# Kernel tuning notes

Hardware: AMD Instinct MI355X
Metric: run time of the kernel (lower is better)

## Reference

```python
import jax, jax.numpy as jnp
import numpy as np

N = 50000
E = 800000
IN_DIM, HID_DIM, LAT_DIM, OUT_DIM = 128, 128, 64, 128
NEG_SLOPE = 0.2  # PyG GATConv default


def setup_inputs() -> dict:
    key = jax.random.key(0)
    ks = jax.random.split(key, 24)
    def glorot(k, shape):
        lim = float(np.sqrt(6.0 / (shape[0] + shape[-1])))
        return jax.random.uniform(k, shape, jnp.float32, -lim, lim)
    inp = {
        "x": jax.random.normal(ks[0], (N, IN_DIM), jnp.float32),
        "edge_index": jax.random.randint(ks[1], (2, E), 0, N, jnp.int32),
        "eps": jax.random.normal(ks[2], (N, LAT_DIM), jnp.float32),
        # GATConv 1 (heads=1)
        "W1": glorot(ks[3], (IN_DIM, HID_DIM)),
        "a_src1": glorot(ks[4], (HID_DIM,)),
        "a_dst1": glorot(ks[5], (HID_DIM,)),
        "b1": jnp.zeros((HID_DIM,), jnp.float32),
        # GATConv 2
        "W2": glorot(ks[6], (HID_DIM, LAT_DIM)),
        "a_src2": glorot(ks[7], (LAT_DIM,)),
        "a_dst2": glorot(ks[8], (LAT_DIM,)),
        "b2": jnp.zeros((LAT_DIM,), jnp.float32),
        # VAE heads
        "W_mu": glorot(ks[9], (LAT_DIM, LAT_DIM)),
        "b_mu": jnp.zeros((LAT_DIM,), jnp.float32),
        "W_lv": glorot(ks[10], (LAT_DIM, LAT_DIM)),
        "b_lv": jnp.zeros((LAT_DIM,), jnp.float32),
        "W_d1": glorot(ks[11], (LAT_DIM, HID_DIM)),
        "b_d1": jnp.zeros((HID_DIM,), jnp.float32),
        "W_d2": glorot(ks[12], (HID_DIM, OUT_DIM)),
        "b_d2": jnp.zeros((OUT_DIM,), jnp.float32),
    }
    return inp


def gat_conv(x, W, a_src, a_dst, b, src, dst):
    # x: [N, F_in] -> h: [N, F_out]
    h = x @ W
    # per-node attention halves (single head)
    alpha_s = h @ a_src           # [N]
    alpha_d = h @ a_dst           # [N]
    # per-edge score: leaky_relu(a_src . h_j + a_dst . h_i), edge j->i
    e = jax.nn.leaky_relu(alpha_s[src] + alpha_d[dst], NEG_SLOPE)  # [E']
    # scatter-softmax over incoming edges of each destination node
    m = jax.ops.segment_max(e, dst, num_segments=N)                # [N]
    ex = jnp.exp(e - m[dst])
    denom = jax.ops.segment_sum(ex, dst, num_segments=N)           # [N]
    w = ex / denom[dst]                                            # [E']
    # scatter-add weighted messages
    out = jax.ops.segment_sum(h[src] * w[:, None], dst, num_segments=N)
    return out + b


def reference(x, edge_index, eps, W1, a_src1, a_dst1, b1, W2, a_src2, a_dst2, b2,
              W_mu, b_mu, W_lv, b_lv, W_d1, b_d1, W_d2, b_d2):
    # add self loops (PyG GATConv default add_self_loops=True)
    loops = jnp.arange(N, dtype=edge_index.dtype)
    src = jnp.concatenate([edge_index[0], loops])
    dst = jnp.concatenate([edge_index[1], loops])

    h = jax.nn.relu(gat_conv(x, W1, a_src1, a_dst1, b1, src, dst))
    h = jax.nn.relu(gat_conv(h, W2, a_src2, a_dst2, b2, src, dst))
    mu = h @ W_mu + b_mu
    logvar = h @ W_lv + b_lv
    z = mu + eps * jnp.exp(0.5 * logvar)
    d = jax.nn.relu(z @ W_d1 + b_d1)
    recon_x = jax.nn.sigmoid(d @ W_d2 + b_d2)
    return recon_x, mu, logvar
```

## Files before the change

kernel.cpp:

```cpp
#include <hip/hip_runtime.h>
#include <stdint.h>

typedef unsigned int u32;

__device__ __forceinline__ float lrelu(float x){ return x > 0.f ? x : 0.2f*x; }

__global__ void k_hist(const int* __restrict__ dst, int* __restrict__ deg, int E){
  int e = blockIdx.x*blockDim.x + threadIdx.x;
  if (e < E) atomicAdd(&deg[dst[e]], 1);
}

__global__ void k_scan1(const int* __restrict__ deg, int* __restrict__ offs,
                        int* __restrict__ bsum, int n){
  __shared__ int lds[256];
  int t = threadIdx.x;
  int base = blockIdx.x*1024 + t*4;
  int v0 = (base+0<n)?deg[base+0]:0;
  int v1 = (base+1<n)?deg[base+1]:0;
  int v2 = (base+2<n)?deg[base+2]:0;
  int v3 = (base+3<n)?deg[base+3]:0;
  int s = v0+v1+v2+v3;
  lds[t] = s; __syncthreads();
  for (int off=1; off<256; off<<=1){
    int tmp = (t>=off)? lds[t-off] : 0;
    __syncthreads();
    lds[t] += tmp;
    __syncthreads();
  }
  int excl = lds[t] - s;
  if (t==255) bsum[blockIdx.x] = lds[255];
  if (base+0<n) offs[base+0] = excl;
  if (base+1<n) offs[base+1] = excl+v0;
  if (base+2<n) offs[base+2] = excl+v0+v1;
  if (base+3<n) offs[base+3] = excl+v0+v1+v2;
}

__global__ void k_scan2(int* bsum, int nb){
  int lane = threadIdx.x;
  int v = (lane<nb)? bsum[lane] : 0;
  int orig = v;
  for (int off=1; off<64; off<<=1){
    int t = __shfl_up(v, off);
    if (lane >= off) v += t;
  }
  if (lane<nb) bsum[lane] = v - orig;
}

__global__ void k_scan3(int* __restrict__ offs, int* __restrict__ cur,
                        const int* __restrict__ bsum, int n){
  int i = blockIdx.x*blockDim.x + threadIdx.x;
  if (i<n){ int v = offs[i] + bsum[i>>10]; offs[i]=v; cur[i]=v; }
}

__global__ void k_scatter(const int* __restrict__ src, const int* __restrict__ dst,
                          int* __restrict__ cur, int* __restrict__ adj, int E){
  int e = blockIdx.x*blockDim.x + threadIdx.x;
  if (e<E){
    int d = dst[e];
    int p = atomicAdd(&cur[d], 1);
    adj[p] = src[e];
  }
}

template<int FOUT>
__global__ void k_gemm(const float* __restrict__ X, const float* __restrict__ W,
                       float* __restrict__ H, int N){
  constexpr int FIN = 128, ROWS = 16;
  __shared__ float xs[ROWS*FIN];
  int t = threadIdx.x;
  long i0 = (long)blockIdx.x*ROWS;
  {
    const float4* xsrc = (const float4*)(X + i0*FIN);
    float4 a = xsrc[t];
    float4 b = xsrc[t+256];
    ((float4*)xs)[t]     = a;
    ((float4*)xs)[t+256] = b;
  }
  __syncthreads();
  constexpr int G = 256/FOUT;
  constexpr int RPT = ROWS/G;
  int c = t % FOUT, g = t / FOUT;
  float acc[RPT];
  #pragma unroll
  for (int r=0;r<RPT;r++) acc[r]=0.f;
  for (int k=0;k<FIN;k+=4){
    float w0 = W[(k+0)*FOUT+c];
    float w1 = W[(k+1)*FOUT+c];
    float w2 = W[(k+2)*FOUT+c];
    float w3 = W[(k+3)*FOUT+c];
    #pragma unroll
    for (int r=0;r<RPT;r++){
      const float4 xv = *(const float4*)&xs[(g*RPT+r)*FIN+k];
      acc[r] = fmaf(xv.w, w3, fmaf(xv.z, w2, fmaf(xv.y, w1, fmaf(xv.x, w0, acc[r]))));
    }
  }
  #pragma unroll
  for (int r=0;r<RPT;r++)
    H[(i0 + g*RPT + r)*FOUT + c] = acc[r];
}

template<int F>
__global__ void k_alpha(const float* __restrict__ H, const float* __restrict__ Asrc,
                        const float* __restrict__ Adst, float* __restrict__ AS,
                        float* __restrict__ AD, int N){
  int lane = threadIdx.x & 63;
  int i = blockIdx.x*4 + (threadIdx.x >> 6);
  if (i >= N) return;
  float as = 0.f, ad = 0.f;
  #pragma unroll
  for (int c = lane; c < F; c += 64){
    float hv = H[(long)i*F + c];
    as = fmaf(hv, Asrc[c], as);
    ad = fmaf(hv, Adst[c], ad);
  }
  #pragma unroll
  for (int off=32; off; off>>=1){
    as += __shfl_xor(as, off);
    ad += __shfl_xor(ad, off);
  }
  if (lane==0){ AS[i]=as; AD[i]=ad; }
}

template<int F>
__global__ void k_agg(const float* __restrict__ H, const float* __restrict__ AS,
                      const float* __restrict__ AD, const float* __restrict__ B,
                      const int* __restrict__ offs, const int* __restrict__ deg,
                      const int* __restrict__ adj, float* __restrict__ OUT, int N){
  int lane = threadIdx.x & 63;
  int i = blockIdx.x*4 + (threadIdx.x >> 6);
  if (i >= N) return;
  int start = offs[i], dg = deg[i];
  float ad = AD[i];
  float lr_self = lrelu(AS[i] + ad);
  float m = -1e30f, dacc = 0.f;
  for (int b0=0; b0<dg; b0+=64){
    int k = b0 + lane;
    if (k < dg){
      int s = adj[start+k];
      float lr = lrelu(AS[s] + ad);
      float mn = fmaxf(m, lr);
      dacc = dacc*__expf(m-mn) + __expf(lr-mn);
      m = mn;
    }
  }
  #pragma unroll
  for (int off=32; off; off>>=1){
    float m2 = __shfl_xor(m, off);
    float d2 = __shfl_xor(dacc, off);
    float mn = fmaxf(m, m2);
    dacc = dacc*__expf(m-mn) + d2*__expf(m2-mn);
    m = mn;
  }
  float M = fmaxf(m, lr_self);
  float D = dacc*__expf(m-M) + __expf(lr_self-M);
  float invD = 1.f/D;
  float wself = __expf(lr_self-M)*invD;
  float acc0 = wself * H[(long)i*F + lane];
  float acc1 = 0.f;
  if (F==128) acc1 = wself * H[(long)i*F + 64 + lane];
  for (int b0=0; b0<dg; b0+=64){
    int k = b0 + lane;
    int sreg = 0; float wreg = 0.f;
    if (k < dg){
      sreg = adj[start+k];
      wreg = __expf(lrelu(AS[sreg]+ad) - M)*invD;
    }
    int cnt = min(64, dg-b0);
    int kk = 0;
    for (; kk+4<=cnt; kk+=4){
      int   s0=__shfl(sreg,kk),   s1=__shfl(sreg,kk+1),   s2=__shfl(sreg,kk+2),   s3=__shfl(sreg,kk+3);
      float w0=__shfl(wreg,kk),   w1=__shfl(wreg,kk+1),   w2=__shfl(wreg,kk+2),   w3=__shfl(wreg,kk+3);
      float h0 = H[(long)s0*F+lane];
      float h1 = H[(long)s1*F+lane];
      float h2 = H[(long)s2*F+lane];
      float h3 = H[(long)s3*F+lane];
      acc0 += w0*h0 + w1*h1 + w2*h2 + w3*h3;
      if (F==128){
        float g0 = H[(long)s0*F+64+lane];
        float g1 = H[(long)s1*F+64+lane];
        float g2 = H[(long)s2*F+64+lane];
        float g3 = H[(long)s3*F+64+lane];
        acc1 += w0*g0 + w1*g1 + w2*g2 + w3*g3;
      }
    }
    for (; kk<cnt; kk++){
      int s0=__shfl(sreg,kk); float w0=__shfl(wreg,kk);
      acc0 += w0*H[(long)s0*F+lane];
      if (F==128) acc1 += w0*H[(long)s0*F+64+lane];
    }
  }
  float o0 = fmaxf(acc0 + B[lane], 0.f);
  OUT[(long)i*F+lane] = o0;
  if (F==128){
    float o1 = fmaxf(acc1 + B[64+lane], 0.f);
    OUT[(long)i*F+64+lane] = o1;
  }
}

__global__ void k_head(const float* __restrict__ H2, const float* __restrict__ EPS,
                       const float* __restrict__ Wmu, const float* __restrict__ bmu,
                       const float* __restrict__ Wlv, const float* __restrict__ blv,
                       const float* __restrict__ Wd1, const float* __restrict__ bd1,
                       const float* __restrict__ Wd2, const float* __restrict__ bd2,
                       float* __restrict__ out_recon, float* __restrict__ out_mu,
                       float* __restrict__ out_lv, int N){
  constexpr int ROWS=16;
  __shared__ float h2s[ROWS*64];
  __shared__ float zs[ROWS*64];
  __shared__ float ds[ROWS*128];
  int t = threadIdx.x;
  long i0 = (long)blockIdx.x*ROWS;
  {
    const float4* s4 = (const float4*)(H2 + i0*64);
    ((float4*)h2s)[t] = s4[t];
  }
  __syncthreads();
  {
    int c = t & 63, q = t >> 6;
    float am[4] = {0,0,0,0}, av[4] = {0,0,0,0};
    for (int k=0;k<64;k++){
      float wm = Wmu[k*64+c];
      float wv = Wlv[k*64+c];
      #pragma unroll
      for (int r=0;r<4;r++){
        float h = h2s[(q*4+r)*64 + k];
        am[r] = fmaf(h, wm, am[r]);
        av[r] = fmaf(h, wv, av[r]);
      }
    }
    float bm = bmu[c], bv = blv[c];
    #pragma unroll
    for (int r=0;r<4;r++){
      int row = q*4+r; long i = i0 + row;
      float mu = am[r] + bm;
      float lv = av[r] + bv;
      out_mu[i*64+c] = mu;
      out_lv[i*64+c] = lv;
      zs[row*64+c] = fmaf(EPS[i*64+c], __expf(0.5f*lv), mu);
    }
  }
  __syncthreads();
  {
    int c = t & 127, q = t >> 7;
    float accd[8] = {0,0,0,0,0,0,0,0};
    for (int k=0;k<64;k++){
      float w = Wd1[k*128+c];
      #pragma unroll
      for (int r=0;r<8;r++)
        accd[r] = fmaf(zs[(q*8+r)*64+k], w, accd[r]);
    }
    float bb = bd1[c];
    #pragma unroll
    for (int r=0;r<8;r++)
      ds[(q*8+r)*128+c] = fmaxf(accd[r]+bb, 0.f);
  }
  __syncthreads();
  {
    int c = t & 127, q = t >> 7;
    float accr[8] = {0,0,0,0,0,0,0,0};
    for (int k=0;k<128;k++){
      float w = Wd2[k*128+c];
      #pragma unroll
      for (int r=0;r<8;r++)
        accr[r] = fmaf(ds[(q*8+r)*128+k], w, accr[r]);
    }
    float bb = bd2[c];
    #pragma unroll
    for (int r=0;r<8;r++){
      long i = i0 + q*8 + r;
      float v = accr[r] + bb;
      out_recon[i*128+c] = 1.f/(1.f+__expf(-v));
    }
  }
}

extern "C" void kernel_launch(void* const* d_in, const int* in_sizes, int n_in,
                              void* d_out, int out_size, void* d_ws, size_t ws_size,
                              hipStream_t stream){
  const float* x    = (const float*)d_in[0];
  const int*   ei   = (const int*)  d_in[1];
  const float* eps  = (const float*)d_in[2];
  const float* W1   = (const float*)d_in[3];
  const float* as1v = (const float*)d_in[4];
  const float* ad1v = (const float*)d_in[5];
  const float* b1   = (const float*)d_in[6];
  const float* W2   = (const float*)d_in[7];
  const float* as2v = (const float*)d_in[8];
  const float* ad2v = (const float*)d_in[9];
  const float* b2   = (const float*)d_in[10];
  const float* Wmu  = (const float*)d_in[11];
  const float* bmu  = (const float*)d_in[12];
  const float* Wlv  = (const float*)d_in[13];
  const float* blv  = (const float*)d_in[14];
  const float* Wd1  = (const float*)d_in[15];
  const float* bd1  = (const float*)d_in[16];
  const float* Wd2  = (const float*)d_in[17];
  const float* bd2  = (const float*)d_in[18];

  const int N = in_sizes[0] / 128;
  const int E = in_sizes[1] / 2;
  const int* esrc = ei;
  const int* edst = ei + E;

  char* wp = (char*)d_ws;
  auto alloc = [&](size_t bytes)->char*{
    char* p = wp; wp += (bytes + 255) & ~(size_t)255; return p;
  };
  int*   deg  = (int*)  alloc((size_t)N*4);
  int*   offs = (int*)  alloc((size_t)N*4);
  int*   cur  = (int*)  alloc((size_t)N*4);
  int*   bsum = (int*)  alloc(256*4);
  int*   adj  = (int*)  alloc((size_t)E*4);
  float* h1   = (float*)alloc((size_t)N*128*4);
  float* o1   = (float*)alloc((size_t)N*128*4);
  float* AS1  = (float*)alloc((size_t)N*4);
  float* AD1  = (float*)alloc((size_t)N*4);
  float* AS2  = (float*)alloc((size_t)N*4);
  float* AD2  = (float*)alloc((size_t)N*4);
  float* h2 = h1;
  float* o2 = h1 + (size_t)N*64;
  (void)ws_size; (void)n_in; (void)out_size;

  float* out_recon = (float*)d_out;
  float* out_mu    = out_recon + (size_t)N*128;
  float* out_lv    = out_mu    + (size_t)N*64;

  hipMemsetAsync(deg, 0, (size_t)N*4, stream);
  int eb = (E + 255)/256;
  int nb = (N + 1023)/1024;
  k_hist   <<<eb, 256, 0, stream>>>(edst, deg, E);
  k_scan1  <<<nb, 256, 0, stream>>>(deg, offs, bsum, N);
  k_scan2  <<<1,   64, 0, stream>>>(bsum, nb);
  k_scan3  <<<(N+255)/256, 256, 0, stream>>>(offs, cur, bsum, N);
  k_scatter<<<eb, 256, 0, stream>>>(esrc, edst, cur, adj, E);

  int gb = N/16;
  int wb = (N+3)/4;
  k_gemm<128> <<<gb, 256, 0, stream>>>(x, W1, h1, N);
  k_alpha<128><<<wb, 256, 0, stream>>>(h1, as1v, ad1v, AS1, AD1, N);
  k_agg<128>  <<<wb, 256, 0, stream>>>(h1, AS1, AD1, b1, offs, deg, adj, o1, N);
  k_gemm<64>  <<<gb, 256, 0, stream>>>(o1, W2, h2, N);
  k_alpha<64> <<<wb, 256, 0, stream>>>(h2, as2v, ad2v, AS2, AD2, N);
  k_agg<64>   <<<wb, 256, 0, stream>>>(h2, AS2, AD2, b2, offs, deg, adj, o2, N);
  k_head      <<<gb, 256, 0, stream>>>(o2, eps, Wmu, bmu, Wlv, blv, Wd1, bd1, Wd2, bd2,
                                       out_recon, out_mu, out_lv, N);
}
```

Before: 443.0 us.

## Register-tile dense GEMMs and VAE head with weights staged in LDS

Rewrites the node-feature GEMM and the fused VAE head so each thread computes a 4-row by 4-column register tile. Weights are staged once per block in shared memory and read as float4, and row tiles grow to 32/64 rows per block. The head now runs with 512 threads and computes mu and logvar together as one 128-wide GEMM. This cuts repeated global weight loads and raises FMA-to-load ratio. In exchange it uses much more LDS per block (about 112KB in the head), which may limit occupancy.

```diff
diff --git a/kernel.cpp b/kernel.cpp
--- a/kernel.cpp
+++ b/kernel.cpp
@@ -63,40 +63,59 @@
 }
 
 template<int FOUT>
-__global__ void k_gemm(const float* __restrict__ X, const float* __restrict__ W,
-                       float* __restrict__ H, int N){
-  constexpr int FIN = 128, ROWS = 16;
-  __shared__ float xs[ROWS*FIN];
+__global__ __launch_bounds__(256) void k_gemm_t(const float* __restrict__ X,
+                                                const float* __restrict__ W,
+                                                float* __restrict__ H, int N){
+  constexpr int CG = FOUT/4;
+  constexpr int RG = 256/CG;
+  constexpr int TR = RG*4;
+  __shared__ float xs[TR*128];
+  __shared__ float ws[128*FOUT];
   int t = threadIdx.x;
-  long i0 = (long)blockIdx.x*ROWS;
-  {
-    const float4* xsrc = (const float4*)(X + i0*FIN);
-    float4 a = xsrc[t];
-    float4 b = xsrc[t+256];
-    ((float4*)xs)[t]     = a;
-    ((float4*)xs)[t+256] = b;
-  }
-  __syncthreads();
-  constexpr int G = 256/FOUT;
-  constexpr int RPT = ROWS/G;
-  int c = t % FOUT, g = t / FOUT;
-  float acc[RPT];
-  #pragma unroll
-  for (int r=0;r<RPT;r++) acc[r]=0.f;
-  for (int k=0;k<FIN;k+=4){
-    float w0 = W[(k+0)*FOUT+c];
-    float w1 = W[(k+1)*FOUT+c];
-    float w2 = W[(k+2)*FOUT+c];
-    float w3 = W[(k+3)*FOUT+c];
-    #pragma unroll
-    for (int r=0;r<RPT;r++){
-      const float4 xv = *(const float4*)&xs[(g*RPT+r)*FIN+k];
-      acc[r] = fmaf(xv.w, w3, fmaf(xv.z, w2, fmaf(xv.y, w1, fmaf(xv.x, w0, acc[r]))));
-    }
-  }
-  #pragma unroll
-  for (int r=0;r<RPT;r++)
-    H[(i0 + g*RPT + r)*FOUT + c] = acc[r];
+  long i0 = (long)blockIdx.x * TR;
+  {
+    constexpr int NV = TR*32/256;
+    #pragma unroll
+    for (int j=0;j<NV;j++){
+      int idx = t + 256*j;
+      int row = idx >> 5, c4 = idx & 31;
+      float4 v = make_float4(0.f,0.f,0.f,0.f);
+      if (i0 + row < N) v = *(const float4*)&X[(i0+row)*128 + c4*4];
+      *(float4*)&xs[row*128 + c4*4] = v;
+    }
+  }
+  {
+    constexpr int NW = 128*FOUT/4/256;
+    const float4* Wv = (const float4*)W;
+    float4* wd = (float4*)ws;
+    #pragma unroll
+    for (int j=0;j<NW;j++) wd[t + 256*j] = Wv[t + 256*j];
+  }
+  __syncthreads();
+  int ci = t & (CG-1), rg = t / CG;
+  float4 a0 = make_float4(0,0,0,0), a1 = a0, a2 = a0, a3 = a0;
+  const float* xrow = &xs[(rg*4)*128];
+  #pragma unroll 8
+  for (int k=0;k<128;k++){
+    float4 w4 = *(const float4*)&ws[k*FOUT + ci*4];
+    float x0 = xrow[k];
+    float x1 = xrow[128 + k];
+    float x2 = xrow[256 + k];
+    float x3 = xrow[384 + k];
+    a0.x = fmaf(x0, w4.x, a0.x); a0.y = fmaf(x0, w4.y, a0.y);
+    a0.z = fmaf(x0, w4.z, a0.z); a0.w = fmaf(x0, w4.w, a0.w);
+    a1.x = fmaf(x1, w4.x, a1.x); a1.y = fmaf(x1, w4.y, a1.y);
+    a1.z = fmaf(x1, w4.z, a1.z); a1.w = fmaf(x1, w4.w, a1.w);
+    a2.x = fmaf(x2, w4.x, a2.x); a2.y = fmaf(x2, w4.y, a2.y);
+    a2.z = fmaf(x2, w4.z, a2.z); a2.w = fmaf(x2, w4.w, a2.w);
+    a3.x = fmaf(x3, w4.x, a3.x); a3.y = fmaf(x3, w4.y, a3.y);
+    a3.z = fmaf(x3, w4.z, a3.z); a3.w = fmaf(x3, w4.w, a3.w);
+  }
+  long ib = i0 + rg*4;
+  if (ib+0 < N) *(float4*)&H[(ib+0)*FOUT + ci*4] = a0;
+  if (ib+1 < N) *(float4*)&H[(ib+1)*FOUT + ci*4] = a1;
+  if (ib+2 < N) *(float4*)&H[(ib+2)*FOUT + ci*4] = a2;
+  if (ib+3 < N) *(float4*)&H[(ib+3)*FOUT + ci*4] = a3;
 }
 
 template<int F>
@@ -197,79 +216,151 @@
   }
 }
 
-__global__ void k_head(const float* __restrict__ H2, const float* __restrict__ EPS,
-                       const float* __restrict__ Wmu, const float* __restrict__ bmu,
-                       const float* __restrict__ Wlv, const float* __restrict__ blv,
-                       const float* __restrict__ Wd1, const float* __restrict__ bd1,
-                       const float* __restrict__ Wd2, const float* __restrict__ bd2,
-                       float* __restrict__ out_recon, float* __restrict__ out_mu,
-                       float* __restrict__ out_lv, int N){
-  constexpr int ROWS=16;
-  __shared__ float h2s[ROWS*64];
-  __shared__ float zs[ROWS*64];
-  __shared__ float ds[ROWS*128];
+__global__ __launch_bounds__(512) void k_head_t(
+    const float* __restrict__ H2, const float* __restrict__ EPS,
+    const float* __restrict__ Wmu, const float* __restrict__ bmu,
+    const float* __restrict__ Wlv, const float* __restrict__ blv,
+    const float* __restrict__ Wd1, const float* __restrict__ bd1,
+    const float* __restrict__ Wd2, const float* __restrict__ bd2,
+    float* __restrict__ out_recon, float* __restrict__ out_mu,
+    float* __restrict__ out_lv, int N){
+  __shared__ float hs[64*64];
+  __shared__ float zs[64*64];
+  __shared__ float dsb[64*128];
+  __shared__ float ws[128*128];
   int t = threadIdx.x;
-  long i0 = (long)blockIdx.x*ROWS;
-  {
-    const float4* s4 = (const float4*)(H2 + i0*64);
-    ((float4*)h2s)[t] = s4[t];
-  }
-  __syncthreads();
-  {
-    int c = t & 63, q = t >> 6;
-    float am[4] = {0,0,0,0}, av[4] = {0,0,0,0};
+  long i0 = (long)blockIdx.x * 64;
+  #pragma unroll
+  for (int j=0;j<2;j++){
+    int idx = t + 512*j;
+    int row = idx >> 4, c4 = idx & 15;
+    float4 v = make_float4(0.f,0.f,0.f,0.f);
+    if (i0 + row < N) v = *(const float4*)&H2[(i0+row)*64 + c4*4];
+    *(float4*)&hs[row*64 + c4*4] = v;
+  }
+  #pragma unroll
+  for (int j=0;j<4;j++){
+    int q = t + 512*j;
+    int k = q >> 5, c4 = q & 31;
+    float4 v;
+    if (c4 < 16) v = *(const float4*)&Wmu[k*64 + c4*4];
+    else         v = *(const float4*)&Wlv[k*64 + (c4-16)*4];
+    *(float4*)&ws[k*128 + c4*4] = v;
+  }
+  __syncthreads();
+  int ci = t & 31, rg = t >> 5;
+  float4 a0 = make_float4(0,0,0,0), a1 = a0, a2 = a0, a3 = a0;
+  {
+    const float* xrow = &hs[(rg*4)*64];
+    #pragma unroll 8
     for (int k=0;k<64;k++){
-      float wm = Wmu[k*64+c];
-      float wv = Wlv[k*64+c];
-      #pragma unroll
-      for (int r=0;r<4;r++){
-        float h = h2s[(q*4+r)*64 + k];
-        am[r] = fmaf(h, wm, am[r]);
-        av[r] = fmaf(h, wv, av[r]);
+      float4 w4 = *(const float4*)&ws[k*128 + ci*4];
+      float x0 = xrow[k], x1 = xrow[64+k], x2 = xrow[128+k], x3 = xrow[192+k];
+      a0.x=fmaf(x0,w4.x,a0.x); a0.y=fmaf(x0,w4.y,a0.y); a0.z=fmaf(x0,w4.z,a0.z); a0.w=fmaf(x0,w4.w,a0.w);
+      a1.x=fmaf(x1,w4.x,a1.x); a1.y=fmaf(x1,w4.y,a1.y); a1.z=fmaf(x1,w4.z,a1.z); a1.w=fmaf(x1,w4.w,a1.w);
+      a2.x=fmaf(x2,w4.x,a2.x); a2.y=fmaf(x2,w4.y,a2.y); a2.z=fmaf(x2,w4.z,a2.z); a2.w=fmaf(x2,w4.w,a2.w);
+      a3.x=fmaf(x3,w4.x,a3.x); a3.y=fmaf(x3,w4.y,a3.y); a3.z=fmaf(x3,w4.z,a3.z); a3.w=fmaf(x3,w4.w,a3.w);
+    }
+  }
+  bool is_mu = (ci < 16);
+  int cbase = is_mu ? ci*4 : (ci-16)*4;
+  if (!is_mu){
+    float4 bv = *(const float4*)&blv[cbase];
+    float4 acc[4] = {a0,a1,a2,a3};
+    #pragma unroll
+    for (int r=0;r<4;r++){
+      long i = i0 + rg*4 + r;
+      float4 lv = make_float4(acc[r].x+bv.x, acc[r].y+bv.y, acc[r].z+bv.z, acc[r].w+bv.w);
+      if (i < N) *(float4*)&out_lv[i*64 + cbase] = lv;
+      *(float4*)&zs[(rg*4+r)*64 + cbase] = lv;
+    }
+  }
+  __syncthreads();
+  if (is_mu){
+    float4 bv = *(const float4*)&bmu[cbase];
+    float4 acc[4] = {a0,a1,a2,a3};
+    #pragma unroll
+    for (int r=0;r<4;r++){
+      long i = i0 + rg*4 + r;
+      float4 mu = make_float4(acc[r].x+bv.x, acc[r].y+bv.y, acc[r].z+bv.z, acc[r].w+bv.w);
+      if (i < N) *(float4*)&out_mu[i*64 + cbase] = mu;
+      float4 lv = *(const float4*)&zs[(rg*4+r)*64 + cbase];
+      float4 e = make_float4(0.f,0.f,0.f,0.f);
+      if (i < N) e = *(const float4*)&EPS[i*64 + cbase];
+      float4 z;
+      z.x = fmaf(e.x, __expf(0.5f*lv.x), mu.x);
+      z.y = fmaf(e.y, __expf(0.5f*lv.y), mu.y);
+      z.z = fmaf(e.z, __expf(0.5f*lv.z), mu.z);
+      z.w = fmaf(e.w, __expf(0.5f*lv.w), mu.w);
+      *(float4*)&zs[(rg*4+r)*64 + cbase] = z;
+    }
+  }
+  {
+    const float4* Wv = (const float4*)Wd1;
+    float4* wd = (float4*)ws;
+    #pragma unroll
+    for (int j=0;j<4;j++) wd[t + 512*j] = Wv[t + 512*j];
+  }
+  __syncthreads();
+  a0 = make_float4(0,0,0,0); a1 = a0; a2 = a0; a3 = a0;
+  {
+    const float* xrow = &zs[(rg*4)*64];
+    #pragma unroll 8
+    for (int k=0;k<64;k++){
+      float4 w4 = *(const float4*)&ws[k*128 + ci*4];
+      float x0 = xrow[k], x1 = xrow[64+k], x2 = xrow[128+k], x3 = xrow[192+k];
+      a0.x=fmaf(x0,w4.x,a0.x); a0.y=fmaf(x0,w4.y,a0.y); a0.z=fmaf(x0,w4.z,a0.z); a0.w=fmaf(x0,w4.w,a0.w);
+      a1.x=fmaf(x1,w4.x,a1.x); a1.y=fmaf(x1,w4.y,a1.y); a1.z=fmaf(x1,w4.z,a1.z); a1.w=fmaf(x1,w4.w,a1.w);
+      a2.x=fmaf(x2,w4.x,a2.x); a2.y=fmaf(x2,w4.y,a2.y); a2.z=fmaf(x2,w4.z,a2.z); a2.w=fmaf(x2,w4.w,a2.w);
+      a3.x=fmaf(x3,w4.x,a3.x); a3.y=fmaf(x3,w4.y,a3.y); a3.z=fmaf(x3,w4.z,a3.z); a3.w=fmaf(x3,w4.w,a3.w);
+    }
+  }
+  __syncthreads();
+  {
+    float4 bv = *(const float4*)&bd1[ci*4];
+    float4 acc[4] = {a0,a1,a2,a3};
+    #pragma unroll
+    for (int r=0;r<4;r++){
+      float4 d;
+      d.x = fmaxf(acc[r].x+bv.x, 0.f); d.y = fmaxf(acc[r].y+bv.y, 0.f);
+      d.z = fmaxf(acc[r].z+bv.z, 0.f); d.w = fmaxf(acc[r].w+bv.w, 0.f);
+      *(float4*)&dsb[(rg*4+r)*128 + ci*4] = d;
+    }
+  }
+  {
+    const float4* Wv = (const float4*)Wd2;
+    float4* wd = (float4*)ws;
+    #pragma unroll
+    for (int j=0;j<8;j++) wd[t + 512*j] = Wv[t + 512*j];
+  }
+  __syncthreads();
+  a0 = make_float4(0,0,0,0); a1 = a0; a2 = a0; a3 = a0;
+  {
+    const float* xrow = &dsb[(rg*4)*128];
+    #pragma unroll 8
+    for (int k=0;k<128;k++){
+      float4 w4 = *(const float4*)&ws[k*128 + ci*4];
+      float x0 = xrow[k], x1 = xrow[128+k], x2 = xrow[256+k], x3 = xrow[384+k];
+      a0.x=fmaf(x0,w4.x,a0.x); a0.y=fmaf(x0,w4.y,a0.y); a0.z=fmaf(x0,w4.z,a0.z); a0.w=fmaf(x0,w4.w,a0.w);
+      a1.x=fmaf(x1,w4.x,a1.x); a1.y=fmaf(x1,w4.y,a1.y); a1.z=fmaf(x1,w4.z,a1.z); a1.w=fmaf(x1,w4.w,a1.w);
+      a2.x=fmaf(x2,w4.x,a2.x); a2.y=fmaf(x2,w4.y,a2.y); a2.z=fmaf(x2,w4.z,a2.z); a2.w=fmaf(x2,w4.w,a2.w);
+      a3.x=fmaf(x3,w4.x,a3.x); a3.y=fmaf(x3,w4.y,a3.y); a3.z=fmaf(x3,w4.z,a3.z); a3.w=fmaf(x3,w4.w,a3.w);
+    }
+  }
+  {
+    float4 bv = *(const float4*)&bd2[ci*4];
+    float4 acc[4] = {a0,a1,a2,a3};
+    #pragma unroll
+    for (int r=0;r<4;r++){
+      long i = i0 + rg*4 + r;
+      if (i < N){
+        float4 o;
+        o.x = 1.f/(1.f+__expf(-(acc[r].x+bv.x)));
+        o.y = 1.f/(1.f+__expf(-(acc[r].y+bv.y)));
+        o.z = 1.f/(1.f+__expf(-(acc[r].z+bv.z)));
+        o.w = 1.f/(1.f+__expf(-(acc[r].w+bv.w)));
+        *(float4*)&out_recon[i*128 + ci*4] = o;
       }
-    }
-    float bm = bmu[c], bv = blv[c];
-    #pragma unroll
-    for (int r=0;r<4;r++){
-      int row = q*4+r; long i = i0 + row;
-      float mu = am[r] + bm;
-      float lv = av[r] + bv;
-      out_mu[i*64+c] = mu;
-      out_lv[i*64+c] = lv;
-      zs[row*64+c] = fmaf(EPS[i*64+c], __expf(0.5f*lv), mu);
-    }
-  }
-  __syncthreads();
-  {
-    int c = t & 127, q = t >> 7;
-    float accd[8] = {0,0,0,0,0,0,0,0};
-    for (int k=0;k<64;k++){
-      float w = Wd1[k*128+c];
-      #pragma unroll
-      for (int r=0;r<8;r++)
-        accd[r] = fmaf(zs[(q*8+r)*64+k], w, accd[r]);
-    }
-    float bb = bd1[c];
-    #pragma unroll
-    for (int r=0;r<8;r++)
-      ds[(q*8+r)*128+c] = fmaxf(accd[r]+bb, 0.f);
-  }
-  __syncthreads();
-  {
-    int c = t & 127, q = t >> 7;
-    float accr[8] = {0,0,0,0,0,0,0,0};
-    for (int k=0;k<128;k++){
-      float w = Wd2[k*128+c];
-      #pragma unroll
-      for (int r=0;r<8;r++)
-        accr[r] = fmaf(ds[(q*8+r)*128+k], w, accr[r]);
-    }
-    float bb = bd2[c];
-    #pragma unroll
-    for (int r=0;r<8;r++){
-      long i = i0 + q*8 + r;
-      float v = accr[r] + bb;
-      out_recon[i*128+c] = 1.f/(1.f+__expf(-v));
     }
   }
 }
@@ -334,14 +425,16 @@
   k_scan3  <<<(N+255)/256, 256, 0, stream>>>(offs, cur, bsum, N);
   k_scatter<<<eb, 256, 0, stream>>>(esrc, edst, cur, adj, E);
 
-  int gb = N/16;
-  int wb = (N+3)/4;
-  k_gemm<128> <<<gb, 256, 0, stream>>>(x, W1, h1, N);
-  k_alpha<128><<<wb, 256, 0, stream>>>(h1, as1v, ad1v, AS1, AD1, N);
-  k_agg<128>  <<<wb, 256, 0, stream>>>(h1, AS1, AD1, b1, offs, deg, adj, o1, N);
-  k_gemm<64>  <<<gb, 256, 0, stream>>>(o1, W2, h2, N);
-  k_alpha<64> <<<wb, 256, 0, stream>>>(h2, as2v, ad2v, AS2, AD2, N);
-  k_agg<64>   <<<wb, 256, 0, stream>>>(h2, AS2, AD2, b2, offs, deg, adj, o2, N);
-  k_head      <<<gb, 256, 0, stream>>>(o2, eps, Wmu, bmu, Wlv, blv, Wd1, bd1, Wd2, bd2,
-                                       out_recon, out_mu, out_lv, N);
-}
+  int wb  = (N+3)/4;
+  int gb1 = (N+31)/32;
+  int gb2 = (N+63)/64;
+  int hb  = (N+63)/64;
+  k_gemm_t<128><<<gb1, 256, 0, stream>>>(x, W1, h1, N);
+  k_alpha<128> <<<wb, 256, 0, stream>>>(h1, as1v, ad1v, AS1, AD1, N);
+  k_agg<128>   <<<wb, 256, 0, stream>>>(h1, AS1, AD1, b1, offs, deg, adj, o1, N);
+  k_gemm_t<64> <<<gb2, 256, 0, stream>>>(o1, W2, h2, N);
+  k_alpha<64>  <<<wb, 256, 0, stream>>>(h2, as2v, ad2v, AS2, AD2, N);
+  k_agg<64>    <<<wb, 256, 0, stream>>>(h2, AS2, AD2, b2, offs, deg, adj, o2, N);
+  k_head_t     <<<hb, 512, 0, stream>>>(o2, eps, Wmu, bmu, Wlv, blv, Wd1, bd1, Wd2, bd2,
+                                        out_recon, out_mu, out_lv, N);
+}
```

Result: no change. 445.4 us (+0.6%).
